# Kernel tuning notes

Hardware: AMD Instinct MI355X
Metric: run time of the kernel (lower is better)

Reference implementation:

```python
import jax, jax.numpy as jnp
import numpy as np

DIM = 256
HEADS = 8
WH, WW = 8, 8
N = WH * WW
B_ = 2048
NW = 64  # num windows per image; B_ // NW = batch of 32
CPB_HIDDEN = 256


def _log_rel_index(wh, ww):
    ch = np.arange(wh)
    cw = np.arange(ww)
    coords = np.stack(np.meshgrid(ch, cw, indexing='ij'))      # (2, wh, ww)
    cf = coords.reshape(2, -1)                                  # (2, N)
    rel = cf[:, :, None] - cf[:, None, :]                       # (2, N, N)
    rel = rel.transpose(1, 2, 0).astype(np.float32)             # (N, N, 2)
    return np.sign(rel) * np.log1p(np.abs(rel))


def setup_inputs() -> dict:
    key = jax.random.key(0)
    ks = jax.random.split(key, 16)
    s = 0.02
    inp = {
        'x': jax.random.normal(ks[0], (B_, N, DIM), jnp.float32),
        'KV': jax.random.normal(ks[1], (B_, N, DIM), jnp.float32),
        'mask': jnp.zeros((NW, N, N), jnp.float32),
        # linear weights stored (in, out): y = x @ W + b
        'Wq': jax.random.normal(ks[2], (DIM, DIM), jnp.float32) * s,
        'bq': jnp.zeros((DIM,), jnp.float32),
        'Wkv': jax.random.normal(ks[3], (DIM, 2 * DIM), jnp.float32) * s,
        'bkv': jnp.zeros((2 * DIM,), jnp.float32),
        'Wp': jax.random.normal(ks[4], (DIM, DIM), jnp.float32) * s,
        'bp': jnp.zeros((DIM,), jnp.float32),
        'cpb_w1': jax.random.normal(ks[5], (2, CPB_HIDDEN), jnp.float32) * s,
        'cpb_b1': jnp.zeros((CPB_HIDDEN,), jnp.float32),
        'cpb_w2': jax.random.normal(ks[6], (CPB_HIDDEN, HEADS), jnp.float32) * s,
        'cpb_b2': jnp.zeros((HEADS,), jnp.float32),
        'tau': jnp.ones((HEADS, N, N), jnp.float32),
        'log_rel_idx': jnp.asarray(_log_rel_index(WH, WW)),  # (N, N, 2)
    }
    return inp


def reference(x, KV, mask, Wq, bq, Wkv, bkv, Wp, bp,
              cpb_w1, cpb_b1, cpb_w2, cpb_b2, tau, log_rel_idx):
    Bw, n, C = x.shape
    H = tau.shape[0]
    hd = C // H
    scale = hd ** -0.5

    q = (x @ Wq + bq).reshape(Bw, n, H, hd).transpose(0, 2, 1, 3) * scale   # (B_,H,N,hd)
    kv = (KV @ Wkv + bkv).reshape(Bw, n, 2, H, hd).transpose(2, 0, 3, 1, 4)  # (2,B_,H,N,hd)
    k, v = kv[0], kv[1]

    num = jnp.einsum('bhqd,bhkd->bhqk', q, k)
    qn = jnp.sqrt(jnp.sum(q * q, axis=-1, keepdims=True))                    # (B_,H,N,1)
    kn = jnp.sqrt(jnp.sum(k * k, axis=-1, keepdims=True))                    # (B_,H,N,1)
    denom = jnp.maximum(qn * kn.transpose(0, 1, 3, 2), 1e-6)
    attn = num / denom
    attn = attn / jnp.clip(tau[:, :n, :n], 0.01)[None]

    # continuous relative position bias MLP: (N,N,2) -> (N,N,H)
    h = jax.nn.relu(log_rel_idx[:n, :n] @ cpb_w1 + cpb_b1)
    bias = (h @ cpb_w2 + cpb_b2).transpose(2, 0, 1)                          # (H,N,N)
    attn = attn + bias[None]

    nW = mask.shape[0]
    attn = attn.reshape(Bw // nW, nW, H, n, n) + mask[None, :, None]
    attn = attn.reshape(Bw, H, n, n)
    attn = jax.nn.softmax(attn, axis=-1)

    out = jnp.einsum('bhqk,bhkd->bhqd', attn, v)
    out = out.transpose(0, 2, 1, 3).reshape(Bw, n, C)
    out = out @ Wp + bp
    return out
```

## Files before the change

kernel.cpp:

```cpp
#include <hip/hip_runtime.h>
#include <hip/hip_bf16.h>

#define NWIN 64

typedef __attribute__((ext_vector_type(8))) short v8s;
typedef __attribute__((ext_vector_type(4))) float v4f;

#define WQT_OFF   0u
#define WKVT_OFF  131072u
#define WPT_OFF   393216u
#define ITB_OFF   524288u

static __device__ __forceinline__ short f2bf(float f) {
  union { float f; unsigned int u; } v; v.f = f;
  unsigned int u = v.u;
  return (short)((u + 0x7fffu + ((u >> 16) & 1u)) >> 16);
}

static __device__ __forceinline__ int packbf(float lo, float hi) {
  __hip_bfloat162 h = __float22bfloat162_rn(float2{lo, hi});
  union { __hip_bfloat162 h; int i; } u; u.h = h; return u.i;
}

__global__ void prep_kernel(const float* __restrict__ Wq, const float* __restrict__ Wkv,
                            const float* __restrict__ Wp, const float* __restrict__ tau,
                            short* __restrict__ WqT, short* __restrict__ WkvT,
                            short* __restrict__ WpT, float2* __restrict__ itb) {
  int id = blockIdx.x * 256 + threadIdx.x;
  if (id < 65536) {
    int o = id >> 8, i = id & 255;
    WqT[id] = f2bf(Wq[i * 256 + o]);
  } else if (id < 196608) {
    int t = id - 65536; int o = t >> 8, i = t & 255;
    WkvT[t] = f2bf(Wkv[i * 512 + o]);
  } else if (id < 262144) {
    int t = id - 196608; int o = t >> 8, i = t & 255;
    WpT[t] = f2bf(Wp[i * 256 + o]);
  } else if (id < 294912) {
    int t = id - 262144;
    itb[t].x = 1.0f / fmaxf(tau[t], 0.01f);
  }
}

__global__ void cpb_kernel(const float* __restrict__ w1, const float* __restrict__ b1,
                           const float* __restrict__ w2, const float* __restrict__ b2,
                           const float* __restrict__ lri, float2* __restrict__ itb) {
  int ij = blockIdx.x * 256 + threadIdx.x;
  float l0 = lri[ij * 2], l1 = lri[ij * 2 + 1];
  float acc[8];
#pragma unroll
  for (int h = 0; h < 8; ++h) acc[h] = b2[h];
  for (int c = 0; c < 256; ++c) {
    float hv = fmaxf(l0 * w1[c] + l1 * w1[256 + c] + b1[c], 0.0f);
#pragma unroll
    for (int h = 0; h < 8; ++h) acc[h] += hv * w2[c * 8 + h];
  }
#pragma unroll
  for (int h = 0; h < 8; ++h) itb[h * 4096 + ij].y = acc[h];
}

static __device__ __forceinline__ v8s xform_tile(int p0a, int p0b, int p1a, int p1b,
                                                 int base, int mdsel) {
  int a0 = __shfl(p0a, base, 64),      b0 = __shfl(p1a, base, 64);
  int a1 = __shfl(p0b, base, 64),      b1 = __shfl(p1b, base, 64);
  int a2 = __shfl(p0a, base + 16, 64), b2 = __shfl(p1a, base + 16, 64);
  int a3 = __shfl(p0b, base + 16, 64), b3 = __shfl(p1b, base + 16, 64);
  union { v8s v; int i[4]; } r;
  r.i[0] = mdsel ? b0 : a0;
  r.i[1] = mdsel ? b1 : a1;
  r.i[2] = mdsel ? b2 : a2;
  r.i[3] = mdsel ? b3 : a3;
  return r.v;
}

__global__ __launch_bounds__(512, 4) void wattn_kernel(
    const float* __restrict__ x, const float* __restrict__ KV,
    const float* __restrict__ mask,
    const float* __restrict__ bq, const float* __restrict__ bkv,
    const float* __restrict__ bp,
    const short* __restrict__ WqT, const short* __restrict__ WkvT,
    const short* __restrict__ WpT, const float2* __restrict__ itb,
    float* __restrict__ out) {
  __shared__ short sm[33792];

  const int b = blockIdx.x;
  const int tid = threadIdx.x;
  const int w = tid >> 6;
  const int lane = tid & 63;
  const int cc = lane & 15;
  const int qd = lane >> 4;
  const int base = cc + 32 * (qd & 1);
  const int mdsel = qd >> 1;
  const v4f vzero = {0.f, 0.f, 0.f, 0.f};
  short* xs = sm;
  short* kvs = sm + 16896;

  {
    const float4* xb = (const float4*)(x + (size_t)b * 16384);
    const float4* kb = (const float4*)(KV + (size_t)b * 16384);
#pragma unroll
    for (int half = 0; half < 2; ++half) {
      float4 vx[4], vk[4];
#pragma unroll
      for (int ii = 0; ii < 4; ++ii) {
        int i = tid + (half * 4 + ii) * 512;
        vx[ii] = xb[i];
        vk[ii] = kb[i];
      }
#pragma unroll
      for (int ii = 0; ii < 4; ++ii) {
        int i = tid + (half * 4 + ii) * 512;
        int r = i >> 6, col = (i & 63) << 2;
        int2 px = { packbf(vx[ii].x, vx[ii].y), packbf(vx[ii].z, vx[ii].w) };
        int2 pk = { packbf(vk[ii].x, vk[ii].y), packbf(vk[ii].z, vk[ii].w) };
        *(int2*)&xs[r * 264 + col] = px;
        *(int2*)&kvs[r * 264 + col] = pk;
      }
    }
  }
  const short* wqb = WqT + (32 * w + cc) * 256 + qd * 8;
  v8s wq0[4], wq1[4];
#pragma unroll
  for (int it = 0; it < 4; ++it) {
    wq0[it] = *(const v8s*)(wqb + it * 32);
    wq1[it] = *(const v8s*)(wqb + 16 * 256 + it * 32);
  }
  __syncthreads();

  v4f Dq[2][4];
#pragma unroll
  for (int md = 0; md < 2; ++md)
#pragma unroll
    for (int nt = 0; nt < 4; ++nt) Dq[md][nt] = vzero;
  {
#pragma unroll
    for (int it = 0; it < 4; ++it) {
#pragma unroll
      for (int nt = 0; nt < 4; ++nt) {
        v8s bx = *(const v8s*)(xs + (nt * 16 + cc) * 264 + it * 32 + qd * 8);
        Dq[0][nt] = __builtin_amdgcn_mfma_f32_16x16x32_bf16(wq0[it], bx, Dq[0][nt], 0, 0, 0);
        Dq[1][nt] = __builtin_amdgcn_mfma_f32_16x16x32_bf16(wq1[it], bx, Dq[1][nt], 0, 0, 0);
      }
    }
#pragma unroll
    for (int it = 4; it < 8; ++it) {
      v8s a0 = *(const v8s*)(wqb + it * 32);
      v8s a1 = *(const v8s*)(wqb + 16 * 256 + it * 32);
#pragma unroll
      for (int nt = 0; nt < 4; ++nt) {
        v8s bx = *(const v8s*)(xs + (nt * 16 + cc) * 264 + it * 32 + qd * 8);
        Dq[0][nt] = __builtin_amdgcn_mfma_f32_16x16x32_bf16(a0, bx, Dq[0][nt], 0, 0, 0);
        Dq[1][nt] = __builtin_amdgcn_mfma_f32_16x16x32_bf16(a1, bx, Dq[1][nt], 0, 0, 0);
      }
    }
  }
  v8s qB[4];
  {
    v4f b0 = *(const v4f*)(bq + 32 * w + qd * 4);
    v4f b1 = *(const v4f*)(bq + 32 * w + 16 + qd * 4);
#pragma unroll
    for (int nt = 0; nt < 4; ++nt) {
      float s = 0.f;
#pragma unroll
      for (int rg = 0; rg < 4; ++rg) {
        float v0 = Dq[0][nt][rg] + b0[rg];
        float v1 = Dq[1][nt][rg] + b1[rg];
        Dq[0][nt][rg] = v0; Dq[1][nt][rg] = v1;
        s += v0 * v0 + v1 * v1;
      }
      s += __shfl_xor(s, 16); s += __shfl_xor(s, 32);
      float inv = rsqrtf(s + 1e-24f);
      int p00 = packbf(Dq[0][nt][0] * inv, Dq[0][nt][1] * inv);
      int p01 = packbf(Dq[0][nt][2] * inv, Dq[0][nt][3] * inv);
      int p10 = packbf(Dq[1][nt][0] * inv, Dq[1][nt][1] * inv);
      int p11 = packbf(Dq[1][nt][2] * inv, Dq[1][nt][3] * inv);
      qB[nt] = xform_tile(p00, p01, p10, p11, base, mdsel);
    }
  }

  v4f Dk[2][4], Dv[4][2];
#pragma unroll
  for (int nt = 0; nt < 4; ++nt) {
    Dk[0][nt] = vzero; Dk[1][nt] = vzero;
    Dv[nt][0] = vzero; Dv[nt][1] = vzero;
  }
  {
    const short* wkb = WkvT + (32 * w + cc) * 256 + qd * 8;
    const short* wvb = WkvT + (256 + 32 * w + cc) * 256 + qd * 8;
#pragma unroll
    for (int it = 0; it < 8; ++it) {
      v8s ak0 = *(const v8s*)(wkb + it * 32);
      v8s ak1 = *(const v8s*)(wkb + 16 * 256 + it * 32);
      v8s bv0 = *(const v8s*)(wvb + it * 32);
      v8s bv1 = *(const v8s*)(wvb + 16 * 256 + it * 32);
#pragma unroll
      for (int nt = 0; nt < 4; ++nt) {
        v8s kf = *(const v8s*)(kvs + (nt * 16 + cc) * 264 + it * 32 + qd * 8);
        Dk[0][nt] = __builtin_amdgcn_mfma_f32_16x16x32_bf16(ak0, kf, Dk[0][nt], 0, 0, 0);
        Dk[1][nt] = __builtin_amdgcn_mfma_f32_16x16x32_bf16(ak1, kf, Dk[1][nt], 0, 0, 0);
        Dv[nt][0] = __builtin_amdgcn_mfma_f32_16x16x32_bf16(kf, bv0, Dv[nt][0], 0, 0, 0);
        Dv[nt][1] = __builtin_amdgcn_mfma_f32_16x16x32_bf16(kf, bv1, Dv[nt][1], 0, 0, 0);
      }
    }
  }
  v8s kA[4];
  {
    v4f b0 = *(const v4f*)(bkv + 32 * w + qd * 4);
    v4f b1 = *(const v4f*)(bkv + 32 * w + 16 + qd * 4);
#pragma unroll
    for (int nt = 0; nt < 4; ++nt) {
      float s = 0.f;
#pragma unroll
      for (int rg = 0; rg < 4; ++rg) {
        float v0 = Dk[0][nt][rg] + b0[rg];
        float v1 = Dk[1][nt][rg] + b1[rg];
        Dk[0][nt][rg] = v0; Dk[1][nt][rg] = v1;
        s += v0 * v0 + v1 * v1;
      }
      s += __shfl_xor(s, 16); s += __shfl_xor(s, 32);
      float inv = rsqrtf(s + 1e-24f);
      int p00 = packbf(Dk[0][nt][0] * inv, Dk[0][nt][1] * inv);
      int p01 = packbf(Dk[0][nt][2] * inv, Dk[0][nt][3] * inv);
      int p10 = packbf(Dk[1][nt][0] * inv, Dk[1][nt][1] * inv);
      int p11 = packbf(Dk[1][nt][2] * inv, Dk[1][nt][3] * inv);
      kA[nt] = xform_tile(p00, p01, p10, p11, base, mdsel);
    }
  }
  v8s av[2][2];
  {
    float bv0 = bkv[256 + 32 * w + cc];
    float bv1 = bkv[256 + 32 * w + 16 + cc];
    int Pv[4][2][2];
#pragma unroll
    for (int vt = 0; vt < 4; ++vt) {
      Pv[vt][0][0] = packbf(Dv[vt][0][0] + bv0, Dv[vt][0][1] + bv0);
      Pv[vt][0][1] = packbf(Dv[vt][0][2] + bv0, Dv[vt][0][3] + bv0);
      Pv[vt][1][0] = packbf(Dv[vt][1][0] + bv1, Dv[vt][1][1] + bv1);
      Pv[vt][1][1] = packbf(Dv[vt][1][2] + bv1, Dv[vt][1][3] + bv1);
    }
#pragma unroll
    for (int md = 0; md < 2; ++md)
#pragma unroll
      for (int kc = 0; kc < 2; ++kc)
        av[md][kc] = xform_tile(Pv[2 * kc][md][0], Pv[2 * kc][md][1],
                                Pv[2 * kc + 1][md][0], Pv[2 * kc + 1][md][1], base, mdsel);
  }

  v4f Sv[4][4];
  __builtin_amdgcn_s_setprio(1);
#pragma unroll
  for (int jt = 0; jt < 4; ++jt)
#pragma unroll
    for (int it = 0; it < 4; ++it)
      Sv[jt][it] = __builtin_amdgcn_mfma_f32_16x16x32_bf16(kA[jt], qB[it], vzero, 0, 0, 0);
  __builtin_amdgcn_s_setprio(0);

  {
    const float4* itb4 = (const float4*)(itb + (size_t)w * 4096);
    const float4* mw4 = (const float4*)(mask + (size_t)(b & (NWIN - 1)) * 4096);
#pragma unroll
    for (int it = 0; it < 4; ++it) {
      int i = it * 16 + cc;
      float4 A[4], Bv[4], Mv[4];
#pragma unroll
      for (int jh = 0; jh < 2; ++jh) {
#pragma unroll
        for (int j2 = 0; j2 < 2; ++j2) {
          int jt = jh * 2 + j2;
          int e = i * 64 + jt * 16 + qd * 4;
          A[jt] = itb4[e >> 1];
          Bv[jt] = itb4[(e >> 1) + 1];
          Mv[jt] = mw4[e >> 2];
        }
#pragma unroll
        for (int j2 = 0; j2 < 2; ++j2) {
          int jt = jh * 2 + j2;
          Sv[jt][it][0] = Sv[jt][it][0] * A[jt].x + A[jt].y + Mv[jt].x;
          Sv[jt][it][1] = Sv[jt][it][1] * A[jt].z + A[jt].w + Mv[jt].y;
          Sv[jt][it][2] = Sv[jt][it][2] * Bv[jt].x + Bv[jt].y + Mv[jt].z;
          Sv[jt][it][3] = Sv[jt][it][3] * Bv[jt].z + Bv[jt].w + Mv[jt].w;
        }
      }
      float mx = -3.4e38f;
#pragma unroll
      for (int jt = 0; jt < 4; ++jt)
#pragma unroll
        for (int rg = 0; rg < 4; ++rg) mx = fmaxf(mx, Sv[jt][it][rg]);
      mx = fmaxf(mx, __shfl_xor(mx, 16)); mx = fmaxf(mx, __shfl_xor(mx, 32));
      float sum = 0.f;
#pragma unroll
      for (int jt = 0; jt < 4; ++jt)
#pragma unroll
        for (int rg = 0; rg < 4; ++rg) {
          float ev = __expf(Sv[jt][it][rg] - mx);
          Sv[jt][it][rg] = ev;
          sum += ev;
        }
      sum += __shfl_xor(sum, 16); sum += __shfl_xor(sum, 32);
      float rs = 1.0f / sum;
#pragma unroll
      for (int jt = 0; jt < 4; ++jt)
#pragma unroll
        for (int rg = 0; rg < 4; ++rg) Sv[jt][it][rg] *= rs;
    }
  }

  __syncthreads();
  v4f Do[2][4];
  {
    char* psw = (char*)kvs + w * 4096;
#pragma unroll
    for (int it = 0; it < 4; ++it) {
      char* ps = psw + (it & 1) * 2048;
#pragma unroll
      for (int jt = 0; jt < 4; ++jt) {
        int2 pr;
        pr.x = packbf(Sv[jt][it][0], Sv[jt][it][1]);
        pr.y = packbf(Sv[jt][it][2], Sv[jt][it][3]);
        int byte = (cc * 128 + jt * 32 + qd * 8) ^ ((cc & 7) << 4);
        *(int2*)(ps + byte) = pr;
      }
      int rb0 = (cc * 128 + qd * 16) ^ ((cc & 7) << 4);
      int rb1 = (cc * 128 + 64 + qd * 16) ^ ((cc & 7) << 4);
      v8s pB0 = *(const v8s*)(ps + rb0);
      v8s pB1 = *(const v8s*)(ps + rb1);
      __builtin_amdgcn_s_setprio(1);
#pragma unroll
      for (int md = 0; md < 2; ++md) {
        v4f t = __builtin_amdgcn_mfma_f32_16x16x32_bf16(av[md][0], pB0, vzero, 0, 0, 0);
        Do[md][it] = __builtin_amdgcn_mfma_f32_16x16x32_bf16(av[md][1], pB1, t, 0, 0, 0);
      }
      __builtin_amdgcn_s_setprio(0);
    }
  }

#pragma unroll
  for (int md = 0; md < 2; ++md)
#pragma unroll
    for (int it = 0; it < 4; ++it) {
      int addr = (it * 16 + cc) * 264 + 32 * w + md * 16 + qd * 4;
      *(int*)&sm[addr] = packbf(Do[md][it][0], Do[md][it][1]);
      *(int*)&sm[addr + 2] = packbf(Do[md][it][2], Do[md][it][3]);
    }
  __syncthreads();

  v4f pa[4][2];
#pragma unroll
  for (int mt = 0; mt < 4; ++mt) { pa[mt][0] = vzero; pa[mt][1] = vzero; }
  {
    const short* wpb = WpT + (32 * w + cc) * 256 + qd * 8;
#pragma unroll
    for (int it = 0; it < 8; ++it) {
      v8s b0 = *(const v8s*)(wpb + it * 32);
      v8s b1 = *(const v8s*)(wpb + 16 * 256 + it * 32);
#pragma unroll
      for (int mt = 0; mt < 4; ++mt) {
        v8s a = *(const v8s*)(sm + (mt * 16 + cc) * 264 + it * 32 + qd * 8);
        pa[mt][0] = __builtin_amdgcn_mfma_f32_16x16x32_bf16(a, b0, pa[mt][0], 0, 0, 0);
        pa[mt][1] = __builtin_amdgcn_mfma_f32_16x16x32_bf16(a, b1, pa[mt][1], 0, 0, 0);
      }
    }
  }
  {
    float b0 = bp[32 * w + cc], b1 = bp[32 * w + 16 + cc];
    float* ob = out + (size_t)b * 16384;
#pragma unroll
    for (int mt = 0; mt < 4; ++mt)
#pragma unroll
      for (int rg = 0; rg < 4; ++rg) {
        int row = mt * 16 + qd * 4 + rg;
        ob[row * 256 + 32 * w + cc] = pa[mt][0][rg] + b0;
        ob[row * 256 + 32 * w + 16 + cc] = pa[mt][1][rg] + b1;
      }
  }
}

extern "C" void kernel_launch(void* const* d_in, const int* in_sizes, int n_in,
                              void* d_out, int out_size, void* d_ws, size_t ws_size,
                              hipStream_t stream) {
  const float* x    = (const float*)d_in[0];
  const float* KV   = (const float*)d_in[1];
  const float* mask = (const float*)d_in[2];
  const float* Wq   = (const float*)d_in[3];
  const float* bq   = (const float*)d_in[4];
  const float* Wkv  = (const float*)d_in[5];
  const float* bkv  = (const float*)d_in[6];
  const float* Wp   = (const float*)d_in[7];
  const float* bp   = (const float*)d_in[8];
  const float* cw1  = (const float*)d_in[9];
  const float* cb1  = (const float*)d_in[10];
  const float* cw2  = (const float*)d_in[11];
  const float* cb2  = (const float*)d_in[12];
  const float* tau  = (const float*)d_in[13];
  const float* lri  = (const float*)d_in[14];

  unsigned char* ws = (unsigned char*)d_ws;
  short* WqT   = (short*)(ws + WQT_OFF);
  short* WkvT  = (short*)(ws + WKVT_OFF);
  short* WpT   = (short*)(ws + WPT_OFF);
  float2* itb  = (float2*)(ws + ITB_OFF);

  prep_kernel<<<1152, 256, 0, stream>>>(Wq, Wkv, Wp, tau, WqT, WkvT, WpT, itb);
  cpb_kernel<<<16, 256, 0, stream>>>(cw1, cb1, cw2, cb2, lri, itb);
  wattn_kernel<<<2048, 512, 0, stream>>>(x, KV, mask, bq, bkv, bp,
                                         WqT, WkvT, WpT, itb, (float*)d_out);
}
```

Before: 550.1 us.

## Pack tau/bias to bf16 pairs, stage mask in LDS, prefetch Wp

The inverse-tau and relative-position bias tables are packed into one 32-bit word per element as two bf16 values, computed in the cpb kernel, which halves the global bytes read per score. The mask tile is loaded at kernel start, converted to bf16 and stored in swizzled shared memory instead of being read from global memory during softmax. The first Wp weight slices are prefetched before the output write, and the max and sum reductions are rebalanced into trees. Rounding tau, bias and mask to bf16 costs precision, and the extra LDS may reduce occupancy.

```diff
diff --git a/kernel.cpp b/kernel.cpp
--- a/kernel.cpp
+++ b/kernel.cpp
@@ -23,9 +23,9 @@
 }
 
 __global__ void prep_kernel(const float* __restrict__ Wq, const float* __restrict__ Wkv,
-                            const float* __restrict__ Wp, const float* __restrict__ tau,
+                            const float* __restrict__ Wp,
                             short* __restrict__ WqT, short* __restrict__ WkvT,
-                            short* __restrict__ WpT, float2* __restrict__ itb) {
+                            short* __restrict__ WpT) {
   int id = blockIdx.x * 256 + threadIdx.x;
   if (id < 65536) {
     int o = id >> 8, i = id & 255;
@@ -36,15 +36,13 @@
   } else if (id < 262144) {
     int t = id - 196608; int o = t >> 8, i = t & 255;
     WpT[t] = f2bf(Wp[i * 256 + o]);
-  } else if (id < 294912) {
-    int t = id - 262144;
-    itb[t].x = 1.0f / fmaxf(tau[t], 0.01f);
   }
 }
 
 __global__ void cpb_kernel(const float* __restrict__ w1, const float* __restrict__ b1,
                            const float* __restrict__ w2, const float* __restrict__ b2,
-                           const float* __restrict__ lri, float2* __restrict__ itb) {
+                           const float* __restrict__ lri, const float* __restrict__ tau,
+                           unsigned int* __restrict__ itbh) {
   int ij = blockIdx.x * 256 + threadIdx.x;
   float l0 = lri[ij * 2], l1 = lri[ij * 2 + 1];
   float acc[8];
@@ -56,7 +54,10 @@
     for (int h = 0; h < 8; ++h) acc[h] += hv * w2[c * 8 + h];
   }
 #pragma unroll
-  for (int h = 0; h < 8; ++h) itb[h * 4096 + ij].y = acc[h];
+  for (int h = 0; h < 8; ++h) {
+    float it = 1.0f / fmaxf(tau[h * 4096 + ij], 0.01f);
+    itbh[h * 4096 + ij] = (unsigned int)packbf(it, acc[h]);
+  }
 }
 
 static __device__ __forceinline__ v8s xform_tile(int p0a, int p0b, int p1a, int p1b,
@@ -79,9 +80,9 @@
     const float* __restrict__ bq, const float* __restrict__ bkv,
     const float* __restrict__ bp,
     const short* __restrict__ WqT, const short* __restrict__ WkvT,
-    const short* __restrict__ WpT, const float2* __restrict__ itb,
+    const short* __restrict__ WpT, const unsigned int* __restrict__ itbh,
     float* __restrict__ out) {
-  __shared__ short sm[33792];
+  __shared__ short sm[37888];
 
   const int b = blockIdx.x;
   const int tid = threadIdx.x;
@@ -94,10 +95,13 @@
   const v4f vzero = {0.f, 0.f, 0.f, 0.f};
   short* xs = sm;
   short* kvs = sm + 16896;
+  short* ms = sm + 33792;
 
   {
     const float4* xb = (const float4*)(x + (size_t)b * 16384);
     const float4* kb = (const float4*)(KV + (size_t)b * 16384);
+    const float4* mb = (const float4*)(mask + (size_t)(b & (NWIN - 1)) * 4096);
+    float4 m0 = mb[tid * 2], m1 = mb[tid * 2 + 1];
 #pragma unroll
     for (int half = 0; half < 2; ++half) {
       float4 vx[4], vk[4];
@@ -117,6 +121,11 @@
         *(int2*)&kvs[r * 264 + col] = pk;
       }
     }
+    int byte = (tid * 16) ^ (((tid >> 3) & 7) << 3);
+    int2 p0 = { packbf(m0.x, m0.y), packbf(m0.z, m0.w) };
+    int2 p1 = { packbf(m1.x, m1.y), packbf(m1.z, m1.w) };
+    *(int2*)((char*)ms + byte) = p0;
+    *(int2*)((char*)ms + (byte ^ 8)) = p1;
   }
   const short* wqb = WqT + (32 * w + cc) * 256 + qd * 8;
   v8s wq0[4], wq1[4];
@@ -256,46 +265,48 @@
   __builtin_amdgcn_s_setprio(0);
 
   {
-    const float4* itb4 = (const float4*)(itb + (size_t)w * 4096);
-    const float4* mw4 = (const float4*)(mask + (size_t)(b & (NWIN - 1)) * 4096);
+    const uint4* th4 = (const uint4*)(itbh + (size_t)w * 4096);
 #pragma unroll
     for (int it = 0; it < 4; ++it) {
       int i = it * 16 + cc;
-      float4 A[4], Bv[4], Mv[4];
-#pragma unroll
-      for (int jh = 0; jh < 2; ++jh) {
-#pragma unroll
-        for (int j2 = 0; j2 < 2; ++j2) {
-          int jt = jh * 2 + j2;
-          int e = i * 64 + jt * 16 + qd * 4;
-          A[jt] = itb4[e >> 1];
-          Bv[jt] = itb4[(e >> 1) + 1];
-          Mv[jt] = mw4[e >> 2];
-        }
-#pragma unroll
-        for (int j2 = 0; j2 < 2; ++j2) {
-          int jt = jh * 2 + j2;
-          Sv[jt][it][0] = Sv[jt][it][0] * A[jt].x + A[jt].y + Mv[jt].x;
-          Sv[jt][it][1] = Sv[jt][it][1] * A[jt].z + A[jt].w + Mv[jt].y;
-          Sv[jt][it][2] = Sv[jt][it][2] * Bv[jt].x + Bv[jt].y + Mv[jt].z;
-          Sv[jt][it][3] = Sv[jt][it][3] * Bv[jt].z + Bv[jt].w + Mv[jt].w;
-        }
-      }
-      float mx = -3.4e38f;
-#pragma unroll
-      for (int jt = 0; jt < 4; ++jt)
-#pragma unroll
-        for (int rg = 0; rg < 4; ++rg) mx = fmaxf(mx, Sv[jt][it][rg]);
+      uint4 T[4]; int2 M[4];
+#pragma unroll
+      for (int jt = 0; jt < 4; ++jt) {
+        T[jt] = th4[(i * 64 + jt * 16 + qd * 4) >> 2];
+        int byte = (i * 128 + jt * 32 + qd * 8) ^ ((i & 7) << 3);
+        M[jt] = *(const int2*)((const char*)ms + byte);
+      }
+#pragma unroll
+      for (int jt = 0; jt < 4; ++jt) {
+        unsigned mxw = (unsigned)M[jt].x, myw = (unsigned)M[jt].y;
+        float m0 = __uint_as_float(mxw << 16);
+        float m1 = __uint_as_float(mxw & 0xffff0000u);
+        float m2 = __uint_as_float(myw << 16);
+        float m3 = __uint_as_float(myw & 0xffff0000u);
+        unsigned u0 = T[jt].x, u1 = T[jt].y, u2 = T[jt].z, u3 = T[jt].w;
+        Sv[jt][it][0] = Sv[jt][it][0] * __uint_as_float(u0 << 16) + (__uint_as_float(u0 & 0xffff0000u) + m0);
+        Sv[jt][it][1] = Sv[jt][it][1] * __uint_as_float(u1 << 16) + (__uint_as_float(u1 & 0xffff0000u) + m1);
+        Sv[jt][it][2] = Sv[jt][it][2] * __uint_as_float(u2 << 16) + (__uint_as_float(u2 & 0xffff0000u) + m2);
+        Sv[jt][it][3] = Sv[jt][it][3] * __uint_as_float(u3 << 16) + (__uint_as_float(u3 & 0xffff0000u) + m3);
+      }
+      float mA = fmaxf(fmaxf(Sv[0][it][0], Sv[0][it][1]), fmaxf(Sv[0][it][2], Sv[0][it][3]));
+      float mB = fmaxf(fmaxf(Sv[1][it][0], Sv[1][it][1]), fmaxf(Sv[1][it][2], Sv[1][it][3]));
+      float mC = fmaxf(fmaxf(Sv[2][it][0], Sv[2][it][1]), fmaxf(Sv[2][it][2], Sv[2][it][3]));
+      float mD = fmaxf(fmaxf(Sv[3][it][0], Sv[3][it][1]), fmaxf(Sv[3][it][2], Sv[3][it][3]));
+      float mx = fmaxf(fmaxf(mA, mB), fmaxf(mC, mD));
       mx = fmaxf(mx, __shfl_xor(mx, 16)); mx = fmaxf(mx, __shfl_xor(mx, 32));
-      float sum = 0.f;
-#pragma unroll
-      for (int jt = 0; jt < 4; ++jt)
-#pragma unroll
-        for (int rg = 0; rg < 4; ++rg) {
-          float ev = __expf(Sv[jt][it][rg] - mx);
-          Sv[jt][it][rg] = ev;
-          sum += ev;
-        }
+      float sj[4];
+#pragma unroll
+      for (int jt = 0; jt < 4; ++jt) {
+        float e0 = __expf(Sv[jt][it][0] - mx);
+        float e1 = __expf(Sv[jt][it][1] - mx);
+        float e2 = __expf(Sv[jt][it][2] - mx);
+        float e3 = __expf(Sv[jt][it][3] - mx);
+        Sv[jt][it][0] = e0; Sv[jt][it][1] = e1;
+        Sv[jt][it][2] = e2; Sv[jt][it][3] = e3;
+        sj[jt] = (e0 + e1) + (e2 + e3);
+      }
+      float sum = (sj[0] + sj[1]) + (sj[2] + sj[3]);
       sum += __shfl_xor(sum, 16); sum += __shfl_xor(sum, 32);
       float rs = 1.0f / sum;
 #pragma unroll
@@ -334,6 +345,14 @@
     }
   }
 
+  const short* wpb = WpT + (32 * w + cc) * 256 + qd * 8;
+  v8s wp0[2], wp1[2];
+#pragma unroll
+  for (int it = 0; it < 2; ++it) {
+    wp0[it] = *(const v8s*)(wpb + it * 32);
+    wp1[it] = *(const v8s*)(wpb + 16 * 256 + it * 32);
+  }
+
 #pragma unroll
   for (int md = 0; md < 2; ++md)
 #pragma unroll
@@ -348,9 +367,17 @@
 #pragma unroll
   for (int mt = 0; mt < 4; ++mt) { pa[mt][0] = vzero; pa[mt][1] = vzero; }
   {
-    const short* wpb = WpT + (32 * w + cc) * 256 + qd * 8;
-#pragma unroll
-    for (int it = 0; it < 8; ++it) {
+#pragma unroll
+    for (int it = 0; it < 2; ++it) {
+#pragma unroll
+      for (int mt = 0; mt < 4; ++mt) {
+        v8s a = *(const v8s*)(sm + (mt * 16 + cc) * 264 + it * 32 + qd * 8);
+        pa[mt][0] = __builtin_amdgcn_mfma_f32_16x16x32_bf16(a, wp0[it], pa[mt][0], 0, 0, 0);
+        pa[mt][1] = __builtin_amdgcn_mfma_f32_16x16x32_bf16(a, wp1[it], pa[mt][1], 0, 0, 0);
+      }
+    }
+#pragma unroll
+    for (int it = 2; it < 8; ++it) {
       v8s b0 = *(const v8s*)(wpb + it * 32);
       v8s b1 = *(const v8s*)(wpb + 16 * 256 + it * 32);
 #pragma unroll
@@ -398,10 +425,10 @@
   short* WqT   = (short*)(ws + WQT_OFF);
   short* WkvT  = (short*)(ws + WKVT_OFF);
   short* WpT   = (short*)(ws + WPT_OFF);
-  float2* itb  = (float2*)(ws + ITB_OFF);
-
-  prep_kernel<<<1152, 256, 0, stream>>>(Wq, Wkv, Wp, tau, WqT, WkvT, WpT, itb);
-  cpb_kernel<<<16, 256, 0, stream>>>(cw1, cb1, cw2, cb2, lri, itb);
+  unsigned int* itbh = (unsigned int*)(ws + ITB_OFF);
+
+  prep_kernel<<<1024, 256, 0, stream>>>(Wq, Wkv, Wp, WqT, WkvT, WpT);
+  cpb_kernel<<<16, 256, 0, stream>>>(cw1, cb1, cw2, cb2, lri, tau, itbh);
   wattn_kernel<<<2048, 512, 0, stream>>>(x, KV, mask, bq, bkv, bp,
-                                         WqT, WkvT, WpT, itb, (float*)d_out);
-}
+                                         WqT, WkvT, WpT, itbh, (float*)d_out);
+}
```

New measurement: 507.7 us. 7.7% less time.
